# Kernel tuning notes

Hardware: AMD Instinct MI355X
Metric: run time of the kernel (lower is better)

Reference implementation:

```python
import jax, jax.numpy as jnp
import numpy as np

RES = 512       # grid resolution per plane
NFEAT = 32      # features per plane level
LRELU_SLOPE = 0.2
PLANE_AXES = ((0, 1), (0, 2), (1, 2))  # NPlaneSum: xy, xz, yz planes


def encode_nplanesum(x_t, planes):
    """x_t: [N,3] in [0,1]; planes: [3,RES,RES,NFEAT]. Bilinear interp on 3 planes, summed."""
    pos = x_t * (RES - 1)                      # [N,3]
    p0f = jnp.floor(pos)
    frac = pos - p0f                           # [N,3]
    p0 = jnp.clip(p0f.astype(jnp.int32), 0, RES - 1)
    p1 = jnp.minimum(p0 + 1, RES - 1)
    h = jnp.zeros((x_t.shape[0], NFEAT), dtype=planes.dtype)
    for k, (a, b) in enumerate(PLANE_AXES):
        pl = planes[k]                         # [RES,RES,NFEAT]
        i0, i1 = p0[:, a], p1[:, a]
        j0, j1 = p0[:, b], p1[:, b]
        fa = frac[:, a:a + 1]
        fb = frac[:, b:b + 1]
        v00 = pl[i0, j0]; v01 = pl[i0, j1]
        v10 = pl[i1, j0]; v11 = pl[i1, j1]
        h = h + (v00 * (1 - fb) + v01 * fb) * (1 - fa) + (v10 * (1 - fb) + v11 * fb) * fa
    return h


def decode_fp16(h, W1, b1, W2, b2):
    """Tiny MLP run in fp16 (as in Decoder), equal_lr scaling = 1/sqrt(fan_in)."""
    s = np.float16(1.0 / np.sqrt(NFEAT))
    y = h.astype(jnp.float16)
    y = jnp.dot(y, W1.astype(jnp.float16) * s) + b1.astype(jnp.float16)
    y = jnp.where(y >= 0, y, jnp.float16(LRELU_SLOPE) * y)   # LeakyReLU(0.2)
    y = jnp.dot(y, W2.astype(jnp.float16) * s) + b2.astype(jnp.float16)
    return y.astype(jnp.float32)                             # [N,4]


def setup_inputs() -> dict:
    key = jax.random.key(0)
    k1, k2, k3, k4 = jax.random.split(key, 4)
    N = 2_097_152
    x = jax.random.uniform(k1, (N, 3), dtype=jnp.float32, minval=-1.0, maxval=1.0)
    planes = jax.random.normal(k2, (3, RES, RES, NFEAT), dtype=jnp.float32) * 0.05
    W1 = jax.random.normal(k3, (NFEAT, NFEAT), dtype=jnp.float32)
    b1 = jnp.zeros((NFEAT,), dtype=jnp.float32)
    W2 = jax.random.normal(k4, (NFEAT, 4), dtype=jnp.float32)
    b2 = jnp.zeros((4,), dtype=jnp.float32)
    return {"x": x, "planes": planes, "W1": W1, "b1": b1, "W2": W2, "b2": b2}


def reference(x, planes, W1, b1, W2, b2):
    # transform_points is identity (K=None); map [-1,1] -> [0,1]
    x_t = (x + 1.0) * 0.5
    h = encode_nplanesum(x_t, planes)
    out = decode_fp16(h, W1, b1, W2, b2)           # [N,4]
    sdf = out[..., 0]
    rgb = (jnp.tanh(out[..., 1:]) + 1.0) * 0.5
    # analytic normals: d(sdf)/d(x_t), matching forward_sdf_nablas
    sdf_sum = lambda xt: decode_fp16(encode_nplanesum(xt, planes), W1, b1, W2, b2)[..., 0].sum()
    nablas = jax.grad(sdf_sum)(x_t)                # [N,3]
    return sdf, h, nablas, rgb
```

## Files before the change

kernel.cpp:

```cpp
#include <hip/hip_runtime.h>
#include <hip/hip_fp16.h>

#define RES 512
#define NF 32

typedef float v2f __attribute__((ext_vector_type(2)));
typedef float v4f __attribute__((ext_vector_type(4)));

static __device__ __forceinline__ float h2f(float v) {
    return __half2float(__float2half(v));
}
static __device__ __forceinline__ v2f mkv2(float a, float b) { v2f r; r.x = a; r.y = b; return r; }
static __device__ __forceinline__ v4f mkv4(float a, float b, float c, float d) {
    v4f r; r.x = a; r.y = b; r.z = c; r.w = d; return r;
}

template <int L>
static __device__ __forceinline__ float qb(float v) {
    return __int_as_float(__builtin_amdgcn_mov_dpp(
        __float_as_int(v), (L | (L << 2) | (L << 4) | (L << 6)), 0xf, 0xf, true));
}
static __device__ __forceinline__ float qsum(float v) {
    v += __int_as_float(__builtin_amdgcn_mov_dpp(__float_as_int(v), 0xB1, 0xf, 0xf, true));
    v += __int_as_float(__builtin_amdgcn_mov_dpp(__float_as_int(v), 0x4E, 0xf, 0xf, true));
    return v;
}

#define GET(v, c) ((c) == 0 ? (v).x : ((c) == 1 ? (v).y : ((c) == 2 ? (v).z : (v).w)))

__global__ __launch_bounds__(256) void stylesdf_fused(
    const float* __restrict__ x,
    const float* __restrict__ planes,
    const float* __restrict__ W1,
    const float* __restrict__ b1,
    const float* __restrict__ W2,
    const float* __restrict__ b2,
    float* __restrict__ out, int N)
{
#pragma clang fp contract(off)
    __shared__ __align__(16) float sW1[NF * NF];
    __shared__ __align__(16) float sW1T[NF * NF];
    __shared__ __align__(16) float sW2[NF * 4];
    __shared__ __align__(16) float sB1[NF];
    __shared__ __align__(16) float sB2[4];
    __shared__ __align__(16) float sW2c0[NF];

    const float S16 = h2f(0.17677669529663687f);
    const float LREL = h2f(0.2f);

    const int tid = threadIdx.x;
    for (int idx = tid; idx < NF * NF; idx += 256) {
        sW1[idx] = h2f(h2f(W1[idx]) * S16);
        sW1T[idx] = h2f(h2f(W1[(idx & 31) * NF + (idx >> 5)]) * S16);
    }
    if (tid < NF * 4) sW2[tid] = h2f(h2f(W2[tid]) * S16);
    if (tid < NF) { sB1[tid] = h2f(b1[tid]); sW2c0[tid] = h2f(h2f(W2[tid * 4]) * S16); }
    if (tid < 4) sB2[tid] = h2f(b2[tid]);
    __syncthreads();

    const int gt = blockIdx.x * 256 + tid;
    const int p = gt >> 2;
    if (p >= N) return;
    const int q = gt & 3;
    const int fq = q << 2;

    float fr0, fr1, fr2;
    int a0lo, a0hi, a1lo, a1hi, a2lo, a2hi;
#define AXIS(c, FR, LO, HI)                                 \
    {                                                       \
        float xt = (x[3 * p + (c)] + 1.0f) * 0.5f;          \
        float pos = xt * 511.0f;                            \
        float pf = floorf(pos);                             \
        FR = pos - pf;                                      \
        int qq = (int)pf;                                   \
        qq = qq < 0 ? 0 : (qq > 511 ? 511 : qq);            \
        LO = qq;                                            \
        HI = (qq + 1 > 511) ? 511 : qq + 1;                 \
    }
    AXIS(0, fr0, a0lo, a0hi)
    AXIS(1, fr1, a1lo, a1hi)
    AXIS(2, fr2, a2lo, a2hi)
#undef AXIS

    const int oA00 = (a0lo * RES + a1lo) << 5, oA01 = (a0lo * RES + a1hi) << 5;
    const int oA10 = (a0hi * RES + a1lo) << 5, oA11 = (a0hi * RES + a1hi) << 5;
    const int oB00 = (a0lo * RES + a2lo) << 5, oB01 = (a0lo * RES + a2hi) << 5;
    const int oB10 = (a0hi * RES + a2lo) << 5, oB11 = (a0hi * RES + a2hi) << 5;
    const int oC00 = (a1lo * RES + a2lo) << 5, oC01 = (a1lo * RES + a2hi) << 5;
    const int oC10 = (a1hi * RES + a2lo) << 5, oC11 = (a1hi * RES + a2hi) << 5;
    const float* pl0 = planes;
    const float* pl1 = planes + RES * RES * NF;
    const float* pl2 = planes + 2 * (RES * RES * NF);

#define LD4(b, off) (*(const float4*)((b) + (off)))

    const float ifa01 = 1.0f - fr0, ifb01 = 1.0f - fr1;
    const float ifa02 = 1.0f - fr0, ifb02 = 1.0f - fr2;
    const float ifa12 = 1.0f - fr1, ifb12 = 1.0f - fr2;

    float hl[8];
    float d0l[8], d1l[8], d2l[8];
    v4f* ho = (v4f*)(out + (size_t)N + (size_t)p * NF);

#pragma unroll
    for (int kk = 0; kk < 2; ++kk) {
        const int fo = fq + 16 * kk;
        const float4 vA00 = LD4(pl0, oA00 + fo), vA01 = LD4(pl0, oA01 + fo);
        const float4 vA10 = LD4(pl0, oA10 + fo), vA11 = LD4(pl0, oA11 + fo);
        const float4 vB00 = LD4(pl1, oB00 + fo), vB01 = LD4(pl1, oB01 + fo);
        const float4 vB10 = LD4(pl1, oB10 + fo), vB11 = LD4(pl1, oB11 + fo);
        const float4 vC00 = LD4(pl2, oC00 + fo), vC01 = LD4(pl2, oC01 + fo);
        const float4 vC10 = LD4(pl2, oC10 + fo), vC11 = LD4(pl2, oC11 + fo);
        float hc[4];
#pragma unroll
        for (int c = 0; c < 4; ++c) {
            const int f = 4 * kk + c;
            {
                const float a00 = GET(vA00, c), a01 = GET(vA01, c);
                const float a10 = GET(vA10, c), a11 = GET(vA11, c);
                const float t4 = (a00 * ifb01 + a01 * fr1) * ifa01;
                const float t8 = (a10 * ifb01 + a11 * fr1) * fr0;
                hc[c] = t4 + t8;
                d0l[f] = (a10 - a00) * ifb01 + (a11 - a01) * fr1;
                d1l[f] = (a01 - a00) * ifa01 + (a11 - a10) * fr0;
            }
            {
                const float a00 = GET(vB00, c), a01 = GET(vB01, c);
                const float a10 = GET(vB10, c), a11 = GET(vB11, c);
                const float t4 = (a00 * ifb02 + a01 * fr2) * ifa02;
                const float t8 = (a10 * ifb02 + a11 * fr2) * fr0;
                hc[c] = (hc[c] + t4) + t8;
                d0l[f] += (a10 - a00) * ifb02 + (a11 - a01) * fr2;
                d2l[f] = (a01 - a00) * ifa02 + (a11 - a10) * fr0;
            }
            {
                const float a00 = GET(vC00, c), a01 = GET(vC01, c);
                const float a10 = GET(vC10, c), a11 = GET(vC11, c);
                const float t4 = (a00 * ifb12 + a01 * fr2) * ifa12;
                const float t8 = (a10 * ifb12 + a11 * fr2) * fr1;
                hc[c] = (hc[c] + t4) + t8;
                d1l[f] += (a10 - a00) * ifb12 + (a11 - a01) * fr2;
                d2l[f] += (a01 - a00) * ifa12 + (a11 - a10) * fr1;
            }
            hl[f] = h2f(hc[c]);
        }
        __builtin_nontemporal_store(mkv4(hc[0], hc[1], hc[2], hc[3]),
                                    &ho[q + 4 * kk]);
    }

    v2f y2[4];
    y2[0] = mkv2(0.f, 0.f); y2[1] = mkv2(0.f, 0.f);
    y2[2] = mkv2(0.f, 0.f); y2[3] = mkv2(0.f, 0.f);

#define YSTEP(half, ow, e)                                                     \
    {                                                                          \
        const int i = 16 * (half) + 4 * (ow) + (e);                            \
        const float hi = qb<(ow)>(hl[(e) + 4 * (half)]);                       \
        const v2f hv = mkv2(hi, hi);                                           \
        const float4 wA = *(const float4*)(sW1 + i * NF + fq);                 \
        const float4 wB = *(const float4*)(sW1 + i * NF + fq + 16);            \
        y2[0] = y2[0] + hv * mkv2(wA.x, wA.y);       \
        y2[1] = y2[1] + hv * mkv2(wA.z, wA.w);                                 \
        y2[2] = y2[2] + hv * mkv2(wB.x, wB.y);                                 \
        y2[3] = y2[3] + hv * mkv2(wB.z, wB.w);                                 \
    }
#define Y4(half, ow) YSTEP(half, ow, 0) YSTEP(half, ow, 1) YSTEP(half, ow, 2) YSTEP(half, ow, 3)
#define Y16(half) Y4(half, 0) Y4(half, 1) Y4(half, 2) Y4(half, 3)
    Y16(0) Y16(1)
#undef Y16
#undef Y4
#undef YSTEP

    float o0 = 0.f, o1 = 0.f, o2 = 0.f, o3 = 0.f;
    float ml[8];
#pragma unroll
    for (int t = 0; t < 8; ++t) {
        const int j = fq + (t & 3) + 16 * (t >> 2);
        const float yt = (t & 1) ? y2[t >> 1].y : y2[t >> 1].x;
        const float yd = h2f(yt);
        const float y16 = h2f(yd + sB1[j]);
        const bool nn = y16 >= 0.0f;
        const float zj = nn ? y16 : h2f(LREL * y16);
        const float4 w2 = ((const float4*)sW2)[j];
        o0 = o0 + zj * w2.x;
        o1 = o1 + zj * w2.y;
        o2 = o2 + zj * w2.z;
        o3 = o3 + zj * w2.w;
        ml[t] = (nn ? 1.0f : LREL) * sW2c0[j];
    }

    v2f g2[4];
    g2[0] = mkv2(0.f, 0.f); g2[1] = mkv2(0.f, 0.f);
    g2[2] = mkv2(0.f, 0.f); g2[3] = mkv2(0.f, 0.f);

#define GSTEP(half, ow, e)                                                     \
    {                                                                          \
        const int j = 16 * (half) + 4 * (ow) + (e);                            \
        const float mj = qb<(ow)>(ml[(e) + 4 * (half)]);                       \
        const v2f mv = mkv2(mj, mj);                                           \
        const float4 wA = *(const float4*)(sW1T + j * NF + fq);                \
        const float4 wB = *(const float4*)(sW1T + j * NF + fq + 16);           \
        g2[0] = __builtin_elementwise_fma(mv, mkv2(wA.x, wA.y), g2[0]);        \
        g2[1] = __builtin_elementwise_fma(mv, mkv2(wA.z, wA.w), g2[1]);        \
        g2[2] = __builtin_elementwise_fma(mv, mkv2(wB.x, wB.y), g2[2]);        \
        g2[3] = __builtin_elementwise_fma(mv, mkv2(wB.z, wB.w), g2[3]);        \
    }
#define G4(half, ow) GSTEP(half, ow, 0) GSTEP(half, ow, 1) GSTEP(half, ow, 2) GSTEP(half, ow, 3)
#define G16(half) G4(half, 0) G4(half, 1) G4(half, 2) G4(half, 3)
    G16(0) G16(1)
#undef G16
#undef G4
#undef GSTEP

    float n0 = 0.f, n1 = 0.f, n2 = 0.f;
#pragma unroll
    for (int t = 0; t < 8; ++t) {
        const float gt_ = (t & 1) ? g2[t >> 1].y : g2[t >> 1].x;
        n0 = fmaf(gt_, d0l[t], n0);
        n1 = fmaf(gt_, d1l[t], n1);
        n2 = fmaf(gt_, d2l[t], n2);
    }

    o0 = qsum(o0); o1 = qsum(o1); o2 = qsum(o2); o3 = qsum(o3);
    n0 = qsum(n0); n1 = qsum(n1); n2 = qsum(n2);

    o0 = h2f(h2f(o0) + sB2[0]);
    o1 = h2f(h2f(o1) + sB2[1]);
    o2 = h2f(h2f(o2) + sB2[2]);
    o3 = h2f(h2f(o3) + sB2[3]);
    n0 *= 511.0f; n1 *= 511.0f; n2 *= 511.0f;

    if (q == 0) __builtin_nontemporal_store(o0, &out[p]);
    if (q == 1) {
        const size_t nb = (size_t)N * 33 + (size_t)p * 3;
        __builtin_nontemporal_store(n0, &out[nb + 0]);
        __builtin_nontemporal_store(n1, &out[nb + 1]);
        __builtin_nontemporal_store(n2, &out[nb + 2]);
    }
    if (q == 2) {
        const size_t rb = (size_t)N * 36 + (size_t)p * 3;
        __builtin_nontemporal_store((tanhf(o1) + 1.0f) * 0.5f, &out[rb + 0]);
        __builtin_nontemporal_store((tanhf(o2) + 1.0f) * 0.5f, &out[rb + 1]);
        __builtin_nontemporal_store((tanhf(o3) + 1.0f) * 0.5f, &out[rb + 2]);
    }
#undef LD4
#undef GET
}

extern "C" void kernel_launch(void* const* d_in, const int* in_sizes, int n_in,
                              void* d_out, int out_size, void* d_ws, size_t ws_size,
                              hipStream_t stream) {
    const float* x      = (const float*)d_in[0];
    const float* planes = (const float*)d_in[1];
    const float* W1     = (const float*)d_in[2];
    const float* b1     = (const float*)d_in[3];
    const float* W2     = (const float*)d_in[4];
    const float* b2     = (const float*)d_in[5];
    float* out = (float*)d_out;
    const int N = in_sizes[0] / 3;
    const long long total = 4LL * N;
    const int blocks = (int)((total + 255) / 256);
    stylesdf_fused<<<blocks, 256, 0, stream>>>(x, planes, W1, b1, W2, b2, out, N);
}
```

Before: 882.9 us.

## Sort points by Morton-ordered grid cell before fused plane-gather kernel

Adds a counting-sort preprocessing pipeline (histogram, scan, scatter) that buckets points into 16x16x16 Morton-ordered cells, then has the fused kernel process points in that order. The goal is better cache locality for the random plane gathers across the three 512x512x32 planes. In exchange it adds four extra kernel launches, atomics over 2M points, and an indirect index load. Outputs are still written at the original point index, so results are unchanged. It only runs if the workspace is large enough.

```diff
diff --git a/kernel.cpp b/kernel.cpp
--- a/kernel.cpp
+++ b/kernel.cpp
@@ -3,6 +3,7 @@
 
 #define RES 512
 #define NF 32
+#define NBINS 4096
 
 typedef float v2f __attribute__((ext_vector_type(2)));
 typedef float v4f __attribute__((ext_vector_type(4)));
@@ -27,6 +28,62 @@
 }
 
 #define GET(v, c) ((c) == 0 ? (v).x : ((c) == 1 ? (v).y : ((c) == 2 ? (v).z : (v).w)))
+
+static __device__ __forceinline__ unsigned part1by2(unsigned v) {
+    v &= 0x3FF;
+    v = (v | v << 16) & 0x30000FF;
+    v = (v | v << 8)  & 0x300F00F;
+    v = (v | v << 4)  & 0x30C30C3;
+    v = (v | v << 2)  & 0x9249249;
+    return v;
+}
+static __device__ __forceinline__ unsigned cellkey(const float* __restrict__ x, int p) {
+    unsigned c[3];
+#pragma unroll
+    for (int a = 0; a < 3; ++a) {
+        float xt = (x[3 * p + a] + 1.0f) * 0.5f;
+        float pos = xt * 511.0f;
+        int q = (int)floorf(pos);
+        q = q < 0 ? 0 : (q > 511 ? 511 : q);
+        c[a] = (unsigned)q >> 5;
+    }
+    return (part1by2(c[0]) << 2) | (part1by2(c[1]) << 1) | part1by2(c[2]);
+}
+
+__global__ void zero_hist(unsigned* __restrict__ h) {
+    h[blockIdx.x * 256 + threadIdx.x] = 0u;
+}
+__global__ void hist_pass(const float* __restrict__ x, unsigned* __restrict__ hist, int N) {
+    for (int p = blockIdx.x * 256 + threadIdx.x; p < N; p += gridDim.x * 256)
+        atomicAdd(&hist[cellkey(x, p)], 1u);
+}
+__global__ void scan_pass(const unsigned* __restrict__ hist, unsigned* __restrict__ cursor) {
+    __shared__ unsigned part[257];
+    const int t = threadIdx.x;
+    unsigned s = 0;
+#pragma unroll
+    for (int i = 0; i < NBINS / 256; ++i) s += hist[t * (NBINS / 256) + i];
+    part[t + 1] = s;
+    if (t == 0) part[0] = 0;
+    __syncthreads();
+    if (t == 0)
+        for (int i = 1; i <= 256; ++i) part[i] += part[i - 1];
+    __syncthreads();
+    unsigned run = part[t];
+    for (int i = 0; i < NBINS / 256; ++i) {
+        const int b = t * (NBINS / 256) + i;
+        const unsigned c = hist[b];
+        cursor[b] = run;
+        run += c;
+    }
+}
+__global__ void scatter_pass(const float* __restrict__ x, unsigned* __restrict__ cursor,
+                             unsigned* __restrict__ order, int N) {
+    for (int p = blockIdx.x * 256 + threadIdx.x; p < N; p += gridDim.x * 256) {
+        const unsigned idx = atomicAdd(&cursor[cellkey(x, p)], 1u);
+        order[idx] = (unsigned)p;
+    }
+}
 
 __global__ __launch_bounds__(256) void stylesdf_fused(
     const float* __restrict__ x,
@@ -35,6 +92,7 @@
     const float* __restrict__ b1,
     const float* __restrict__ W2,
     const float* __restrict__ b2,
+    const unsigned* __restrict__ order,
     float* __restrict__ out, int N)
 {
 #pragma clang fp contract(off)
@@ -59,8 +117,9 @@
     __syncthreads();
 
     const int gt = blockIdx.x * 256 + tid;
-    const int p = gt >> 2;
-    if (p >= N) return;
+    const int gq = gt >> 2;
+    if (gq >= N) return;
+    const int p = order ? (int)order[gq] : gq;
     const int q = gt & 3;
     const int fq = q << 2;
 
@@ -258,7 +317,20 @@
     const float* b2     = (const float*)d_in[5];
     float* out = (float*)d_out;
     const int N = in_sizes[0] / 3;
+
+    const size_t needed = (size_t)(2 * NBINS + N) * sizeof(unsigned);
+    unsigned* order = nullptr;
+    if (d_ws && ws_size >= needed) {
+        unsigned* hist   = (unsigned*)d_ws;
+        unsigned* cursor = hist + NBINS;
+        order            = cursor + NBINS;
+        zero_hist<<<NBINS / 256, 256, 0, stream>>>(hist);
+        hist_pass<<<2048, 256, 0, stream>>>(x, hist, N);
+        scan_pass<<<1, 256, 0, stream>>>(hist, cursor);
+        scatter_pass<<<2048, 256, 0, stream>>>(x, cursor, order, N);
+    }
+
     const long long total = 4LL * N;
     const int blocks = (int)((total + 255) / 256);
-    stylesdf_fused<<<blocks, 256, 0, stream>>>(x, planes, W1, b1, W2, b2, out, N);
-}
+    stylesdf_fused<<<blocks, 256, 0, stream>>>(x, planes, W1, b1, W2, b2, order, out, N);
+}
```

Result: slower. 1.236 ms (+40.0%).
